# Optimization experiments

Hardware: AMD Instinct MI355X
Metric: run time of the kernel (lower is better)

## Reference

```python
import jax, jax.numpy as jnp
import numpy as np

EPS = 1e-8

def _cosine(a, b):
    # a: (b,h,s,d), b: (b,1,1,d) -> (b,h,s). torch eps semantics: clamp each norm.
    num = jnp.sum(a * b, axis=-1)
    na = jnp.maximum(jnp.linalg.norm(a, axis=-1), EPS)
    nb = jnp.maximum(jnp.linalg.norm(b, axis=-1), EPS)
    return num / (na * nb)

def setup_inputs() -> dict:
    B, H, S, DH, DM = 2, 16, 2048, 64, 1024
    key = jax.random.key(0)
    ks = jax.random.split(key, 8)
    queries = jax.random.normal(ks[0], (B, H, S, DH), dtype=jnp.float32)
    keys = jax.random.normal(ks[1], (B, H, S, DH), dtype=jnp.float32)
    context = jax.random.normal(ks[2], (B, DM), dtype=jnp.float32)
    prev_state = jax.random.normal(ks[3], (B, S, DH), dtype=jnp.float32)
    # causal mask (1 = keep, 0 = masked), shape (B,1,S,S)
    attention_mask = jnp.broadcast_to(jnp.tril(jnp.ones((S, S), dtype=jnp.int32)), (B, 1, S, S))
    # learned params (Linear weights stored torch-style as (out, in))
    cfm_ctx_w = jax.random.normal(ks[4], (DH, DM), dtype=jnp.float32) / np.sqrt(DM)
    cfm_state_w = jax.random.normal(ks[5], (DH, DH), dtype=jnp.float32) / np.sqrt(DH)
    afm_ctx_w = jax.random.normal(ks[6], (DH, DM), dtype=jnp.float32) / np.sqrt(DM)
    cfm_scale = jnp.full((1,), 0.1, dtype=jnp.float32)
    afm_scale = jnp.full((1,), 0.1, dtype=jnp.float32)
    alpha = jnp.asarray(0.1, dtype=jnp.float32)
    beta = jnp.asarray(0.1, dtype=jnp.float32)
    return dict(queries=queries, keys=keys, context=context, prev_state=prev_state,
                attention_mask=attention_mask, cfm_ctx_w=cfm_ctx_w, cfm_state_w=cfm_state_w,
                cfm_scale=cfm_scale, afm_ctx_w=afm_ctx_w, afm_scale=afm_scale,
                alpha=alpha, beta=beta)

def reference(queries, keys, context, prev_state, attention_mask,
              cfm_ctx_w, cfm_state_w, cfm_scale, afm_ctx_w, afm_scale, alpha, beta):
    B, H, S, DH = queries.shape
    # QK^T / sqrt(d_k): (b,h,s,s)
    attn_scores = jnp.einsum('bhqd,bhkd->bhqk', queries, keys) / jnp.sqrt(jnp.asarray(DH, queries.dtype))
    # ---- CFM ----
    cfm_ctx = (context @ cfm_ctx_w.T)[:, None, None, :]            # (b,1,1,dh)
    witt = _cosine(keys, cfm_ctx)                                   # (b,h,s)
    state = (prev_state @ cfm_state_w.T)[:, None, :, :]             # (b,1,s,dh)
    hamming = jnp.mean(((keys > 0) != (state > 0)).astype(keys.dtype), axis=-1)  # (b,h,s)
    cfm = ((witt + (1.0 - hamming)) * cfm_scale[0])[:, :, None, :]  # (b,h,1,s)
    # ---- AFM (no key_probs -> uniform entropy 1/S) ----
    afm_ctx = (context @ afm_ctx_w.T)[:, None, None, :]
    contradiction = jax.nn.relu(-_cosine(keys, afm_ctx))            # (b,h,s)
    entropy = jnp.full_like(contradiction, 1.0 / S)
    afm = ((contradiction + entropy) * afm_scale[0])[:, :, None, :]
    composite = attn_scores + alpha * cfm - beta * afm
    composite = jnp.where(attention_mask == 0, -jnp.inf, composite)
    return composite
```

## Files before the change

kernel.cpp:

```cpp
#include <hip/hip_runtime.h>
#include <math.h>

#define BB 2
#define HH 16
#define SS 2048
#define DHD 64
#define DMD 1024
#define EPSF 1e-8f
#define NEG_FILL -1.0e30f

typedef __attribute__((ext_vector_type(8))) short bf16x8;
typedef __attribute__((ext_vector_type(4))) float f32x4;

#define WS_BIAS_F   1024
#define WS_CONV_F   66560
#define CONV_ELEMS  (BB * HH * SS * DHD)
#define GRAN_TOTAL  (CONV_ELEMS / 8)
#define WS_NEEDED_B ((size_t)WS_CONV_F * 4 + (size_t)CONV_ELEMS * 2 * 4)

static __device__ __forceinline__ unsigned short f2bf(float f) {
    unsigned u = __float_as_uint(f);
    u += 0x7FFFu + ((u >> 16) & 1u);
    return (unsigned short)(u >> 16);
}
static __device__ __forceinline__ float bf2f(unsigned short h) {
    return __uint_as_float(((unsigned)h) << 16);
}
static __device__ __forceinline__ void cvt8(const float* p, bf16x8& h8, bf16x8& l8) {
    float4 v0 = *(const float4*)p;
    float4 v1 = *(const float4*)(p + 4);
    float vf[8] = {v0.x, v0.y, v0.z, v0.w, v1.x, v1.y, v1.z, v1.w};
    #pragma unroll
    for (int j = 0; j < 8; ++j) {
        unsigned short h = f2bf(vf[j]);
        h8[j] = (short)h;
        l8[j] = (short)f2bf(vf[j] - bf2f(h));
    }
}

__global__ void ctx_kernel(const float* __restrict__ context,
                           const float* __restrict__ cfm_ctx_w,
                           const float* __restrict__ afm_ctx_w,
                           float* __restrict__ ws) {
    int t = threadIdx.x;
    int b = t >> 7, sel = (t >> 6) & 1, o = t & 63;
    const float* W = sel ? afm_ctx_w : cfm_ctx_w;
    const float4* wrow = (const float4*)(W + o * DMD);
    const float4* crow = (const float4*)(context + b * DMD);
    float acc = 0.f;
    for (int m = 0; m < DMD / 4; ++m) {
        float4 w4 = wrow[m];
        float4 c4 = crow[m];
        acc += w4.x * c4.x + w4.y * c4.y + w4.z * c4.z + w4.w * c4.w;
    }
    ws[b * 128 + sel * 64 + o] = acc;
    float sq = acc * acc;
    for (int off = 32; off >= 1; off >>= 1) sq += __shfl_xor(sq, off);
    if (o == 0) ws[256 + b * 2 + sel] = fmaxf(sqrtf(sq), EPSF);
}

__global__ void bias_kernel(const float* __restrict__ keys,
                            const float* __restrict__ prev_state,
                            const float* __restrict__ cfm_state_w,
                            const float* __restrict__ cfm_scale,
                            const float* __restrict__ afm_scale,
                            const float* __restrict__ alpha_p,
                            const float* __restrict__ beta_p,
                            const float* __restrict__ ws_ctx,
                            float* __restrict__ bias_out) {
    int gid = blockIdx.x * 4 + (threadIdx.x >> 6);
    int b = gid >> 11, s = gid & (SS - 1);
    int l = threadIdx.x & 63;
    const float4* prow = (const float4*)(prev_state + ((size_t)b * SS + s) * DHD);
    const float4* wrow = (const float4*)(cfm_state_w + l * DHD);
    float st = 0.f;
    #pragma unroll
    for (int j = 0; j < DHD / 4; ++j) {
        float4 p4 = prow[j], w4 = wrow[j];
        st += p4.x * w4.x + p4.y * w4.y + p4.z * w4.z + p4.w * w4.w;
    }
    unsigned long long smask = __ballot(st > 0.f);

    int h = l >> 2, q = l & 3, d0 = q * 16;
    int sb = (int)((smask >> d0) & 0xFFFFull);
    const float* krow = keys + (((size_t)(b * HH + h)) * SS + s) * DHD + d0;
    const float* cc = ws_ctx + b * 128 + d0;
    const float* ac = ws_ctx + b * 128 + 64 + d0;
    float v0 = 0.f, v1 = 0.f, v2 = 0.f, mism = 0.f;
    #pragma unroll
    for (int j4 = 0; j4 < 4; ++j4) {
        float4 k4 = *(const float4*)(krow + j4 * 4);
        float4 c4 = *(const float4*)(cc + j4 * 4);
        float4 a4 = *(const float4*)(ac + j4 * 4);
        float kf[4] = {k4.x, k4.y, k4.z, k4.w};
        float cf[4] = {c4.x, c4.y, c4.z, c4.w};
        float af[4] = {a4.x, a4.y, a4.z, a4.w};
        #pragma unroll
        for (int j = 0; j < 4; ++j) {
            float kd = kf[j];
            v0 = fmaf(kd, cf[j], v0);
            v1 = fmaf(kd, af[j], v1);
            v2 = fmaf(kd, kd, v2);
            int bit = (sb >> (j4 * 4 + j)) & 1;
            mism += ((kd > 0.f) != (bit != 0)) ? 1.f : 0.f;
        }
    }
    v0 += __shfl_xor(v0, 1); v0 += __shfl_xor(v0, 2);
    v1 += __shfl_xor(v1, 1); v1 += __shfl_xor(v1, 2);
    v2 += __shfl_xor(v2, 1); v2 += __shfl_xor(v2, 2);
    mism += __shfl_xor(mism, 1); mism += __shfl_xor(mism, 2);
    if (q == 0) {
        float nb_c = ws_ctx[256 + b * 2];
        float nb_a = ws_ctx[256 + b * 2 + 1];
        float al = alpha_p[0] * cfm_scale[0];
        float be = beta_p[0] * afm_scale[0];
        float nk = fmaxf(sqrtf(v2), EPSF);
        float witt = v0 / (nk * nb_c);
        float contra = fmaxf(-(v1 / (nk * nb_a)), 0.f);
        float ham = mism * (1.f / 64.f);
        bias_out[(size_t)(b * HH + h) * SS + s] =
            al * (witt + 1.f - ham) - be * (contra + 1.f / (float)SS);
    }
}

__global__ void conv_kernel(const float* __restrict__ Q,
                            const float* __restrict__ K,
                            unsigned short* __restrict__ wsc) {
    int sel = blockIdx.y;
    const float* src = sel ? K : Q;
    float scale = sel ? 1.f : 0.125f;
    unsigned short* hi = wsc + (size_t)(sel ? 2 : 0) * CONV_ELEMS;
    unsigned short* lo = hi + CONV_ELEMS;
    int gid = blockIdx.x * 256 + threadIdx.x;
    int bh = gid >> 14;
    int rem = gid & 16383;
    int u = rem >> 7, r2 = rem & 127;
    int s = r2 >> 6, r3 = r2 & 63;
    int lg = r3 >> 4, lr = r3 & 15;
    size_t sidx = ((size_t)bh * SS + u * 16 + lr) * DHD + s * 32 + lg * 8;
    float4 a = *(const float4*)(src + sidx);
    float4 b = *(const float4*)(src + sidx + 4);
    float vf[8] = {a.x, a.y, a.z, a.w, b.x, b.y, b.z, b.w};
    bf16x8 h8, l8;
    #pragma unroll
    for (int j = 0; j < 8; ++j) {
        float f = vf[j] * scale;
        unsigned short h = f2bf(f);
        h8[j] = (short)h;
        l8[j] = (short)f2bf(f - bf2f(h));
    }
    *(bf16x8*)(hi + (size_t)gid * 8) = h8;
    *(bf16x8*)(lo + (size_t)gid * 8) = l8;
}

#define MFMA16(A, B, C) __builtin_amdgcn_mfma_f32_16x16x32_bf16(A, B, C, 0, 0, 0)

__global__ __launch_bounds__(256, 2) void band_pc(
    const unsigned short* __restrict__ wsc,
    const float* __restrict__ bias, float* __restrict__ out) {
    int L = blockIdx.x;
    int xcd = L & 7, sL = L >> 3;
    int j = sL & 31;
    int bh = ((sL >> 5) << 3) | xcd;
    int tid = threadIdx.x;
    int w = tid >> 6, l = tid & 63, lr = l & 15, lg = l >> 4;
    int lg4 = lg * 4;

    int nchunks = (131 - 2 * j) >> 2;
    int mcA = (2 * j + 5) >> 2;

    __shared__ unsigned short KB[2][8192];
    __shared__ float BIASL[2048];

    const unsigned short* Qh = wsc;
    const unsigned short* Ql = Qh + CONV_ELEMS;
    const unsigned short* Kh = Ql + CONV_ELEMS;
    const unsigned short* Kl = Kh + CONV_ELEMS;
    const float* bias_g = bias + (size_t)bh * SS;
    float* ob = out + (size_t)bh * SS * SS;
    size_t kbase = (size_t)bh * 131072;

#define STAGE(cidx, nb) do {                                                 \
    bf16x8 t[8];                                                             \
    _Pragma("unroll")                                                        \
    for (int gi = 0; gi < 8; ++gi) {                                         \
        int g = pw * 8 + gi, u = g >> 2, q = g & 3;                          \
        const unsigned short* src = (q < 2 ? Kh : Kl) + kbase                \
            + (size_t)((cidx) * 4 + u) * 1024 + (q & 1) * 512 + l * 8;       \
        t[gi] = *(const bf16x8*)src;                                         \
    }                                                                        \
    _Pragma("unroll")                                                        \
    for (int gi = 0; gi < 8; ++gi) {                                         \
        int g = pw * 8 + gi, u = g >> 2, q = g & 3;                          \
        *(bf16x8*)&KB[nb][u * 2048 + q * 512 + l * 8] = t[gi];               \
    }                                                                        \
} while (0)

    if (w >= 2) {
        int pw = w - 2;
        #pragma unroll
        for (int i = 0; i < 4; ++i) {
            f32x4 bv = *(const f32x4*)(bias_g + pw * 1024 + i * 256 + l * 4);
            *(f32x4*)&BIASL[pw * 1024 + i * 256 + l * 4] = bv;
        }
        STAGE(0, 0);
        asm volatile("s_waitcnt lgkmcnt(0)" ::: "memory");
        __builtin_amdgcn_sched_barrier(0);
        for (int c = 0; c < nchunks; ++c) {
            __builtin_amdgcn_s_barrier();
            if (c + 1 < nchunks) {
                STAGE(c + 1, (c + 1) & 1);
                asm volatile("s_waitcnt lgkmcnt(0)" ::: "memory");
                __builtin_amdgcn_sched_barrier(0);
            }
        }
    } else {
        int row0 = (w == 0) ? j * 32 : (63 - j) * 32;
        int mych = (w == 0) ? mcA : nchunks;
        bf16x8 q0h0, q0h1, q0l0, q0l1, q1h0, q1h1, q1l0, q1l1;
        {
            size_t qb = kbase + (size_t)(row0 >> 4) * 1024;
            q0h0 = *(const bf16x8*)(Qh + qb + l * 8);
            q0h1 = *(const bf16x8*)(Qh + qb + 512 + l * 8);
            q1h0 = *(const bf16x8*)(Qh + qb + 1024 + l * 8);
            q1h1 = *(const bf16x8*)(Qh + qb + 1536 + l * 8);
            q0l0 = *(const bf16x8*)(Ql + qb + l * 8);
            q0l1 = *(const bf16x8*)(Ql + qb + 512 + l * 8);
            q1l0 = *(const bf16x8*)(Ql + qb + 1024 + l * 8);
            q1l1 = *(const bf16x8*)(Ql + qb + 1536 + l * 8);
        }
        for (int c = 0; c < nchunks; ++c) {
            __builtin_amdgcn_s_barrier();
            if (c < mych) {
                const unsigned short* kb = &KB[c & 1][0];
                #pragma unroll
                for (int u = 0; u < 4; ++u) {
                    int ug = c * 4 + u;
                    bf16x8 kh0 = *(const bf16x8*)&kb[u * 2048 + l * 8];
                    bf16x8 kh1 = *(const bf16x8*)&kb[u * 2048 + 512 + l * 8];
                    bf16x8 kl0 = *(const bf16x8*)&kb[u * 2048 + 1024 + l * 8];
                    bf16x8 kl1 = *(const bf16x8*)&kb[u * 2048 + 1536 + l * 8];
                    f32x4 bv = *(const f32x4*)&BIASL[ug * 16 + lg4];
                    int c0 = ug * 16 + lg4;
                    {
                        int row = row0 + lr;
                        f32x4 a = {0.f, 0.f, 0.f, 0.f};
                        a = MFMA16(kh0, q0h0, a);
                        a = MFMA16(kh1, q0h1, a);
                        a = MFMA16(kh0, q0l0, a);
                        a = MFMA16(kh1, q0l1, a);
                        a = MFMA16(kl0, q0h0, a);
                        a = MFMA16(kl1, q0h1, a);
                        f32x4 v;
                        #pragma unroll
                        for (int e = 0; e < 4; ++e) {
                            float x = a[e] + bv[e];
                            if (c0 + e > row) x = NEG_FILL;
                            v[e] = x;
                        }
                        __builtin_nontemporal_store(v,
                            (f32x4*)(ob + (size_t)row * SS + c0));
                    }
                    {
                        int row = row0 + 16 + lr;
                        f32x4 a = {0.f, 0.f, 0.f, 0.f};
                        a = MFMA16(kh0, q1h0, a);
                        a = MFMA16(kh1, q1h1, a);
                        a = MFMA16(kh0, q1l0, a);
                        a = MFMA16(kh1, q1l1, a);
                        a = MFMA16(kl0, q1h0, a);
                        a = MFMA16(kl1, q1h1, a);
                        f32x4 v;
                        #pragma unroll
                        for (int e = 0; e < 4; ++e) {
                            float x = a[e] + bv[e];
                            if (c0 + e > row) x = NEG_FILL;
                            v[e] = x;
                        }
                        __builtin_nontemporal_store(v,
                            (f32x4*)(ob + (size_t)row * SS + c0));
                    }
                }
            }
        }
    }

    {
        int fillA = mcA * 64, fillZ = nchunks * 64;
        f32x4 f4 = {NEG_FILL, NEG_FILL, NEG_FILL, NEG_FILL};
        for (int r = w; r < 64; r += 4) {
            int grow = (r < 32) ? (j * 32 + r) : ((63 - j) * 32 + (r - 32));
            int f0 = (r < 32) ? fillA : fillZ;
            float* orow = ob + (size_t)grow * SS;
            for (int cc = f0 + l * 4; cc < SS; cc += 256)
                __builtin_nontemporal_store(f4, (f32x4*)(orow + cc));
        }
    }
#undef STAGE
}

#define LOADB(S, unit) do {                                                  \
    size_t _r = ((size_t)bh * SS + (unit) * 16 + lr) * DHD + lg * 8;         \
    cvt8(K + _r, S##h0, S##l0);                                              \
    cvt8(K + _r + 32, S##h1, S##l1);                                         \
    S##bv = *(const f32x4*)(bias_row + (unit) * 16 + lg4);                   \
} while (0)

#define COMP(S, unit) do {                                                   \
    int _c0 = (unit) * 16 + lg4;                                             \
    {                                                                        \
        int _row = row0 + lr;                                                \
        f32x4 _a = {0.f, 0.f, 0.f, 0.f};                                     \
        _a = MFMA16(S##h0, q0h0, _a);                                        \
        _a = MFMA16(S##h1, q0h1, _a);                                        \
        _a = MFMA16(S##h0, q0l0, _a);                                        \
        _a = MFMA16(S##h1, q0l1, _a);                                        \
        _a = MFMA16(S##l0, q0h0, _a);                                        \
        _a = MFMA16(S##l1, q0h1, _a);                                        \
        f32x4 _v;                                                            \
        _Pragma("unroll")                                                    \
        for (int _e = 0; _e < 4; ++_e) {                                     \
            float _x = fmaf(_a[_e], 0.125f, S##bv[_e]);                      \
            if (_c0 + _e > _row) _x = NEG_FILL;                              \
            _v[_e] = _x;                                                     \
        }                                                                    \
        __builtin_nontemporal_store(_v, (f32x4*)(ob + (size_t)_row * SS + _c0)); \
    }                                                                        \
    {                                                                        \
        int _row = row0 + 16 + lr;                                           \
        f32x4 _a = {0.f, 0.f, 0.f, 0.f};                                     \
        _a = MFMA16(S##h0, q1h0, _a);                                        \
        _a = MFMA16(S##h1, q1h1, _a);                                        \
        _a = MFMA16(S##h0, q1l0, _a);                                        \
        _a = MFMA16(S##h1, q1l1, _a);                                        \
        _a = MFMA16(S##l0, q1h0, _a);                                        \
        _a = MFMA16(S##l1, q1h1, _a);                                        \
        f32x4 _v;                                                            \
        _Pragma("unroll")                                                    \
        for (int _e = 0; _e < 4; ++_e) {                                     \
            float _x = fmaf(_a[_e], 0.125f, S##bv[_e]);                      \
            if (_c0 + _e > _row) _x = NEG_FILL;                              \
            _v[_e] = _x;                                                     \
        }                                                                    \
        __builtin_nontemporal_store(_v, (f32x4*)(ob + (size_t)_row * SS + _c0)); \
    }                                                                        \
} while (0)

__global__ __launch_bounds__(128, 2) void band_fallback(
    const float* __restrict__ Q, const float* __restrict__ K,
    const float* __restrict__ bias, float* __restrict__ out) {
    int L = blockIdx.x;
    int xcd = L & 7, sL = L >> 3;
    int j = sL & 31;
    int bh = ((sL >> 5) << 3) | xcd;
    int tid = threadIdx.x;
    int w = tid >> 6, l = tid & 63, lr = l & 15, lg = l >> 4;
    int lg4 = lg * 4;
    int band = w ? (63 - j) : j;
    int row0 = band * 32;
    int nunits = 2 * band + 2;

    const float* bias_row = bias + (size_t)bh * SS;
    float* ob = out + (size_t)bh * SS * SS;

    bf16x8 q0h0, q0h1, q0l0, q0l1, q1h0, q1h1, q1l0, q1l1;
    {
        size_t qr0 = ((size_t)bh * SS + row0 + lr) * DHD + lg * 8;
        cvt8(Q + qr0, q0h0, q0l0);
        cvt8(Q + qr0 + 32, q0h1, q0l1);
        size_t qr1 = qr0 + (size_t)16 * DHD;
        cvt8(Q + qr1, q1h0, q1l0);
        cvt8(Q + qr1 + 32, q1h1, q1l1);
    }

    bf16x8 Ah0, Ah1, Al0, Al1, Bh0, Bh1, Bl0, Bl1;
    f32x4 Abv, Bbv;
    LOADB(A, 0);
    LOADB(B, 1);
    for (int u = 0; u < nunits; u += 2) {
        COMP(A, u);
        if (u + 2 < nunits) LOADB(A, u + 2);
        COMP(B, u + 1);
        if (u + 3 < nunits) LOADB(B, u + 3);
    }

    f32x4 f4 = {NEG_FILL, NEG_FILL, NEG_FILL, NEG_FILL};
    int fill0 = nunits * 16;
    for (int r = 0; r < 32; ++r) {
        float* orow = ob + (size_t)(row0 + r) * SS;
        for (int c = fill0 + l * 4; c < SS; c += 256)
            __builtin_nontemporal_store(f4, (f32x4*)(orow + c));
    }
}

extern "C" void kernel_launch(void* const* d_in, const int* in_sizes, int n_in,
                              void* d_out, int out_size, void* d_ws, size_t ws_size,
                              hipStream_t stream) {
    const float* queries     = (const float*)d_in[0];
    const float* keys        = (const float*)d_in[1];
    const float* context     = (const float*)d_in[2];
    const float* prev_state  = (const float*)d_in[3];
    const float* cfm_ctx_w   = (const float*)d_in[5];
    const float* cfm_state_w = (const float*)d_in[6];
    const float* cfm_scale   = (const float*)d_in[7];
    const float* afm_ctx_w   = (const float*)d_in[8];
    const float* afm_scale   = (const float*)d_in[9];
    const float* alpha_p     = (const float*)d_in[10];
    const float* beta_p      = (const float*)d_in[11];
    float* out = (float*)d_out;
    float* ws  = (float*)d_ws;
    float* bias = ws + WS_BIAS_F;
    unsigned short* wsc = (unsigned short*)(ws + WS_CONV_F);

    ctx_kernel<<<1, 256, 0, stream>>>(context, cfm_ctx_w, afm_ctx_w, ws);
    bias_kernel<<<BB * SS / 4, 256, 0, stream>>>(keys, prev_state, cfm_state_w,
                                                 cfm_scale, afm_scale, alpha_p,
                                                 beta_p, ws, bias);
    if (ws_size >= WS_NEEDED_B) {
        conv_kernel<<<dim3(GRAN_TOTAL / 256, 2), 256, 0, stream>>>(
            queries, keys, wsc);
        band_pc<<<1024, 256, 0, stream>>>(wsc, bias, out);
    } else {
        band_fallback<<<1024, 128, 0, stream>>>(queries, keys, bias, out);
    }
}
```

Measured before the change: 231.0 us.

## Stage MFMA outputs through swizzled LDS to emit full-row coalesced stores

```diff
diff --git a/kernel.cpp b/kernel.cpp
--- a/kernel.cpp
+++ b/kernel.cpp
@@ -166,11 +166,17 @@
     int w = tid >> 6, l = tid & 63, lr = l & 15, lg = l >> 4;
     int lg4 = lg * 4;
 
-    int nchunks = (131 - 2 * j) >> 2;
-    int mcA = (2 * j + 5) >> 2;
+    int chunksA = (j >> 1) + 1;
+    int chunksA4 = (chunksA + 3) & ~3;
+    int chunksZ = 32 - (j >> 1);
+    int chunksZ4 = chunksZ + 3 > 32 ? 32 : ((chunksZ + 3) & ~3);
+    if (chunksZ4 > 32) chunksZ4 = 32;
+    int nchunks = chunksZ4;
+    int ngroups = nchunks >> 2;
 
     __shared__ unsigned short KB[2][8192];
     __shared__ float BIASL[2048];
+    __shared__ float TR[2][16 * 256];
 
     const unsigned short* Qh = wsc;
     const unsigned short* Ql = Qh + CONV_ELEMS;
@@ -216,7 +222,8 @@
         }
     } else {
         int row0 = (w == 0) ? j * 32 : (63 - j) * 32;
-        int mych = (w == 0) ? mcA : nchunks;
+        int mygroups = ((w == 0) ? chunksA4 : chunksZ4) >> 2;
+        float* trw = &TR[w][0];
         bf16x8 q0h0, q0h1, q0l0, q0l1, q1h0, q1h1, q1l0, q1l1;
         {
             size_t qb = kbase + (size_t)(row0 >> 4) * 1024;
@@ -229,64 +236,94 @@
             q1l0 = *(const bf16x8*)(Ql + qb + 1024 + l * 8);
             q1l1 = *(const bf16x8*)(Ql + qb + 1536 + l * 8);
         }
-        for (int c = 0; c < nchunks; ++c) {
-            __builtin_amdgcn_s_barrier();
-            if (c < mych) {
-                const unsigned short* kb = &KB[c & 1][0];
-                #pragma unroll
-                for (int u = 0; u < 4; ++u) {
-                    int ug = c * 4 + u;
-                    bf16x8 kh0 = *(const bf16x8*)&kb[u * 2048 + l * 8];
-                    bf16x8 kh1 = *(const bf16x8*)&kb[u * 2048 + 512 + l * 8];
-                    bf16x8 kl0 = *(const bf16x8*)&kb[u * 2048 + 1024 + l * 8];
-                    bf16x8 kl1 = *(const bf16x8*)&kb[u * 2048 + 1536 + l * 8];
-                    f32x4 bv = *(const f32x4*)&BIASL[ug * 16 + lg4];
-                    int c0 = ug * 16 + lg4;
-                    {
-                        int row = row0 + lr;
-                        f32x4 a = {0.f, 0.f, 0.f, 0.f};
-                        a = MFMA16(kh0, q0h0, a);
-                        a = MFMA16(kh1, q0h1, a);
-                        a = MFMA16(kh0, q0l0, a);
-                        a = MFMA16(kh1, q0l1, a);
-                        a = MFMA16(kl0, q0h0, a);
-                        a = MFMA16(kl1, q0h1, a);
-                        f32x4 v;
-                        #pragma unroll
-                        for (int e = 0; e < 4; ++e) {
-                            float x = a[e] + bv[e];
-                            if (c0 + e > row) x = NEG_FILL;
-                            v[e] = x;
+        f32x4 acc0[16], acc1[16];
+        for (int g = 0; g < ngroups; ++g) {
+            if (g < mygroups) {
+                #pragma unroll
+                for (int cc = 0; cc < 4; ++cc) {
+                    __builtin_amdgcn_s_barrier();
+                    const unsigned short* kb = &KB[cc & 1][0];
+                    #pragma unroll
+                    for (int u = 0; u < 4; ++u) {
+                        int ui = cc * 4 + u;
+                        int ug = g * 16 + ui;
+                        bf16x8 kh0 = *(const bf16x8*)&kb[u * 2048 + l * 8];
+                        bf16x8 kh1 = *(const bf16x8*)&kb[u * 2048 + 512 + l * 8];
+                        bf16x8 kl0 = *(const bf16x8*)&kb[u * 2048 + 1024 + l * 8];
+                        bf16x8 kl1 = *(const bf16x8*)&kb[u * 2048 + 1536 + l * 8];
+                        f32x4 bv = *(const f32x4*)&BIASL[ug * 16 + lg4];
+                        int c0 = ug * 16 + lg4;
+                        {
+                            int row = row0 + lr;
+                            f32x4 a = {0.f, 0.f, 0.f, 0.f};
+                            a = MFMA16(kh0, q0h0, a);
+                            a = MFMA16(kh1, q0h1, a);
+                            a = MFMA16(kh0, q0l0, a);
+                            a = MFMA16(kh1, q0l1, a);
+                            a = MFMA16(kl0, q0h0, a);
+                            a = MFMA16(kl1, q0h1, a);
+                            #pragma unroll
+                            for (int e = 0; e < 4; ++e) {
+                                float x = a[e] + bv[e];
+                                if (c0 + e > row) x = NEG_FILL;
+                                a[e] = x;
+                            }
+                            acc0[ui] = a;
                         }
-                        __builtin_nontemporal_store(v,
-                            (f32x4*)(ob + (size_t)row * SS + c0));
-                    }
-                    {
-                        int row = row0 + 16 + lr;
-                        f32x4 a = {0.f, 0.f, 0.f, 0.f};
-                        a = MFMA16(kh0, q1h0, a);
-                        a = MFMA16(kh1, q1h1, a);
-                        a = MFMA16(kh0, q1l0, a);
-                        a = MFMA16(kh1, q1l1, a);
-                        a = MFMA16(kl0, q1h0, a);
-                        a = MFMA16(kl1, q1h1, a);
-                        f32x4 v;
-                        #pragma unroll
-                        for (int e = 0; e < 4; ++e) {
-                            float x = a[e] + bv[e];
-                            if (c0 + e > row) x = NEG_FILL;
-                            v[e] = x;
+                        {
+                            int row = row0 + 16 + lr;
+                            f32x4 a = {0.f, 0.f, 0.f, 0.f};
+                            a = MFMA16(kh0, q1h0, a);
+                            a = MFMA16(kh1, q1h1, a);
+                            a = MFMA16(kh0, q1l0, a);
+                            a = MFMA16(kh1, q1l1, a);
+                            a = MFMA16(kl0, q1h0, a);
+                            a = MFMA16(kl1, q1h1, a);
+                            #pragma unroll
+                            for (int e = 0; e < 4; ++e) {
+                                float x = a[e] + bv[e];
+                                if (c0 + e > row) x = NEG_FILL;
+                                a[e] = x;
+                            }
+                            acc1[ui] = a;
                         }
-                        __builtin_nontemporal_store(v,
-                            (f32x4*)(ob + (size_t)row * SS + c0));
                     }
                 }
+                #pragma unroll
+                for (int u16 = 0; u16 < 16; ++u16)
+                    *(f32x4*)&trw[lr * 256 + ((u16 * 16 + lg4) ^ ((lr & 7) << 2))] = acc0[u16];
+                asm volatile("s_waitcnt lgkmcnt(0)" ::: "memory");
+                __builtin_amdgcn_sched_barrier(0);
+                #pragma unroll
+                for (int r = 0; r < 16; ++r) {
+                    f32x4 v = *(const f32x4*)&trw[r * 256 + ((l * 4) ^ ((r & 7) << 2))];
+                    __builtin_nontemporal_store(v,
+                        (f32x4*)(ob + (size_t)(row0 + r) * SS + g * 256 + l * 4));
+                }
+                asm volatile("s_waitcnt lgkmcnt(0)" ::: "memory");
+                __builtin_amdgcn_sched_barrier(0);
+                #pragma unroll
+                for (int u16 = 0; u16 < 16; ++u16)
+                    *(f32x4*)&trw[lr * 256 + ((u16 * 16 + lg4) ^ ((lr & 7) << 2))] = acc1[u16];
+                asm volatile("s_waitcnt lgkmcnt(0)" ::: "memory");
+                __builtin_amdgcn_sched_barrier(0);
+                #pragma unroll
+                for (int r = 0; r < 16; ++r) {
+                    f32x4 v = *(const f32x4*)&trw[r * 256 + ((l * 4) ^ ((r & 7) << 2))];
+                    __builtin_nontemporal_store(v,
+                        (f32x4*)(ob + (size_t)(row0 + 16 + r) * SS + g * 256 + l * 4));
+                }
+                asm volatile("s_waitcnt lgkmcnt(0)" ::: "memory");
+                __builtin_amdgcn_sched_barrier(0);
+            } else {
+                #pragma unroll
+                for (int cc = 0; cc < 4; ++cc) __builtin_amdgcn_s_barrier();
             }
         }
     }
 
     {
-        int fillA = mcA * 64, fillZ = nchunks * 64;
+        int fillA = chunksA4 * 64, fillZ = chunksZ4 * 64;
         f32x4 f4 = {NEG_FILL, NEG_FILL, NEG_FILL, NEG_FILL};
         for (int r = w; r < 64; r += 4) {
             int grow = (r < 32) ? (j * 32 + r) : ((63 - j) * 32 + (r - 32));
```

New measurement: 204.6 us. 11.4% less time.
